# Kernel tuning notes

Hardware: AMD Instinct MI355X
Metric: run time of the kernel (lower is better)

The kernel has to match this reference:

```python
import jax, jax.numpy as jnp
import numpy as np
from jax import lax

WINDOW = 8
MAX_VAL = 1.0
C1 = (0.01 * MAX_VAL) ** 2
C2 = (0.03 * MAX_VAL) ** 2


def _box_sum(x):
    # Equivalent to conv2d with an all-ones WINDOW x WINDOW kernel, groups=C, VALID padding.
    return lax.reduce_window(x, 0.0, lax.add,
                             window_dimensions=(1, 1, WINDOW, WINDOW),
                             window_strides=(1, 1, 1, 1),
                             padding='VALID')


def setup_inputs() -> dict:
    key = jax.random.key(0)
    k1, k2 = jax.random.split(key)
    shape = (32, 3, 512, 512)  # NCHW, C=3 per groups=3 conv
    groundtruth = jax.random.uniform(k1, shape, dtype=jnp.float32)
    noisy_img = jax.random.uniform(k2, shape, dtype=jnp.float32)
    return {"groundtruth": groundtruth, "noisy_img": noisy_img}


def reference(groundtruth, noisy_img):
    mu1 = _box_sum(groundtruth)
    mu2 = _box_sum(noisy_img)
    mu1_sq = mu1 * mu1
    mu2_sq = mu2 * mu2
    mu1_mu2 = mu1 * mu2
    sigma1_sq = _box_sum(groundtruth * groundtruth) - mu1_sq
    sigma2_sq = _box_sum(noisy_img * noisy_img) - mu2_sq
    sigma12 = _box_sum(groundtruth * noisy_img) - mu1_mu2
    ssim_map = ((2.0 * mu1_mu2 + C1) * (2.0 * sigma12 + C2)) / (
        (mu1_sq + mu2_sq + C1) * (sigma1_sq + sigma2_sq + C2))
    return jnp.mean(1.0 - ssim_map)
```

## Files before the change

### kernel.cpp

```cpp
#include <hip/hip_runtime.h>


#define W 512
#define H 512
#define OW 505
#define OH 505
#define TH 16
#define NSTRIP ((OH + TH - 1) / TH)
#define NIMG 96
#define NPIX (96.0 * 505.0 * 505.0)

__device__ __forceinline__ float4 ld4(const float* p) { return *(const float4*)p; }
__device__ __forceinline__ float4 f4add(float4 a, float4 b) {
    return make_float4(a.x + b.x, a.y + b.y, a.z + b.z, a.w + b.w);
}
__device__ __forceinline__ float4 f4sub(float4 a, float4 b) {
    return make_float4(a.x - b.x, a.y - b.y, a.z - b.z, a.w - b.w);
}
__device__ __forceinline__ float4 f4mul(float4 a, float4 b) {
    return make_float4(a.x * b.x, a.y * b.y, a.z * b.z, a.w * b.w);
}

__global__ void finalize(const double* p, float* out) {
    out[0] = 1.0f - (float)(*p / NPIX);
}

__global__ void __launch_bounds__(128, 2)
ssim_main(const float* __restrict__ gt, const float* __restrict__ ni,
          double* __restrict__ acc_out)
{
    const int t   = threadIdx.x;
    const int c0  = t * 4;
    const int img = blockIdx.y;
    const int R0  = blockIdx.x * TH;
    const int R1  = min(R0 + TH, OH);

    const float C1 = 1e-4f;
    const float C2 = 9e-4f;

    const float* gx = gt + (size_t)img * (W * H) + c0;
    const float* gy = ni + (size_t)img * (W * H) + c0;

    __shared__ float vbuf[2][4][520];
    __shared__ float wpart[2];

    float4 ring_x[8], ring_y[8];
    float4 vsx = make_float4(0, 0, 0, 0);
    float4 vsy = make_float4(0, 0, 0, 0);
    float4 vsq = make_float4(0, 0, 0, 0);
    float4 vsp = make_float4(0, 0, 0, 0);

#pragma unroll
    for (int k = 0; k < 7; ++k) {
        float4 x = ld4(gx + (size_t)(R0 + k) * W);
        float4 y = ld4(gy + (size_t)(R0 + k) * W);
        ring_x[k] = x; ring_y[k] = y;
        vsx = f4add(vsx, x);
        vsy = f4add(vsy, y);
        vsq = f4add(vsq, f4add(f4mul(x, x), f4mul(y, y)));
        vsp = f4add(vsp, f4mul(x, y));
    }
    ring_x[7] = make_float4(0, 0, 0, 0);
    ring_y[7] = make_float4(0, 0, 0, 0);

    float4 px = ld4(gx + (size_t)(R0 + 7) * W);
    float4 py = ld4(gy + (size_t)(R0 + 7) * W);

    float acc = 0.0f;

#define HORIZ(q, v) {                                                     \
        float4 n1 = *(float4*)&vbuf[b][q][c0 + 4];                        \
        float4 n2 = *(float4*)&vbuf[b][q][c0 + 8];                        \
        float s = ((v.x + v.y) + (v.z + v.w)) +                           \
                  ((n1.x + n1.y) + (n1.z + n1.w));                        \
        B[q][0] = s;                                                      \
        s += n2.x - v.x; B[q][1] = s;                                     \
        s += n2.y - v.y; B[q][2] = s;                                     \
        s += n2.z - v.z; B[q][3] = s;                                     \
    }

#define ROWBODY(k, slot) {                                                \
        const int r = rbase + (k);                                        \
        if (r < R1) {                                  \
            float4 cx = px, cy = py;    \
            float4 ox = ring_x[slot], oy = ring_y[slot];                  \
            vsx = f4add(f4sub(vsx, ox), cx);                              \
            vsy = f4add(f4sub(vsy, oy), cy);                              \
            vsq = f4add(vsq, f4sub(f4add(f4mul(cx, cx), f4mul(cy, cy)),   \
                                   f4add(f4mul(ox, ox), f4mul(oy, oy)))); \
            vsp = f4add(vsp, f4sub(f4mul(cx, cy), f4mul(ox, oy)));        \
            ring_x[slot] = cx; ring_y[slot] = cy;                         \
            const int b = r & 1;                                          \
            *(float4*)&vbuf[b][0][c0] = vsx;                              \
            *(float4*)&vbuf[b][1][c0] = vsy;                              \
            *(float4*)&vbuf[b][2][c0] = vsq;                              \
            *(float4*)&vbuf[b][3][c0] = vsp;                              \
            __syncthreads();                                              \
            if (r + 1 < R1) {  \
                px = ld4(gx + (size_t)(r + 8) * W);                       \
                py = ld4(gy + (size_t)(r + 8) * W);                       \
            }                                                             \
            float B[4][4];                                                \
            HORIZ(0, vsx); HORIZ(1, vsy); HORIZ(2, vsq); HORIZ(3, vsp);   \
            _Pragma("unroll")                                             \
            for (int j = 0; j < 4; ++j) {                                 \
                float Sx = B[0][j], Sy = B[1][j];                         \
                float Sq = B[2][j], Sp = B[3][j];                         \
                float mu12 = Sx * Sy;                                     \
                float n1v = 2.0f * mu12 + C1;                             \
                float n2v = 2.0f * (Sp - mu12) + C2;                      \
                float sx2 = Sx * Sx, sy2 = Sy * Sy;                       \
                float d1  = sx2 + sy2 + C1;                               \
                float d2  = (Sq - sx2 - sy2) + C2;                        \
                float sv  = (n1v * n2v) * __builtin_amdgcn_rcpf(d1 * d2); \
                if (c0 + j < OW) acc += sv;                               \
            }                                                             \
        }                                                                 \
    }

    for (int rbase = R0; rbase < R1; rbase += 8) {
        ROWBODY(0, 7)
        ROWBODY(1, 0)
        ROWBODY(2, 1)
        ROWBODY(3, 2)
        ROWBODY(4, 3)
        ROWBODY(5, 4)
        ROWBODY(6, 5)
        ROWBODY(7, 6)
    }

#pragma unroll
    for (int off = 32; off > 0; off >>= 1) acc += __shfl_down(acc, off);
    const int wave = t >> 6, lane = t & 63;
    if (lane == 0) wpart[wave] = acc;
    __syncthreads();
    if (t == 0) atomicAdd(acc_out, (double)(wpart[0] + wpart[1]));
}

extern "C" void kernel_launch(void* const* d_in, const int* in_sizes, int n_in,
                              void* d_out, int out_size, void* d_ws, size_t ws_size,
                              hipStream_t stream) {
    const float* gt = (const float*)d_in[0];
    const float* ni = (const float*)d_in[1];
    double* acc = (double*)d_ws;

    hipMemsetAsync(acc, 0, sizeof(double), stream);
    dim3 grid(NSTRIP, NIMG);
    ssim_main<<<grid, 128, 0, stream>>>(gt, ni, acc);
    finalize<<<1, 1, 0, stream>>>(acc, (float*)d_out);
}
```

Baseline: 232.9 us.

## Batch four rows per barrier and deepen global prefetch to four rows

Result: no change. 229.4 us (-1.5%).

```diff
diff --git a/kernel.cpp b/kernel.cpp
--- a/kernel.cpp
+++ b/kernel.cpp
@@ -41,7 +41,7 @@
     const float* gx = gt + (size_t)img * (W * H) + c0;
     const float* gy = ni + (size_t)img * (W * H) + c0;
 
-    __shared__ float vbuf[2][4][520];
+    __shared__ float vbuf[4][4][520];
     __shared__ float wpart[2];
 
     float4 ring_x[8], ring_y[8];
@@ -63,26 +63,18 @@
     ring_x[7] = make_float4(0, 0, 0, 0);
     ring_y[7] = make_float4(0, 0, 0, 0);
 
-    float4 px = ld4(gx + (size_t)(R0 + 7) * W);
-    float4 py = ld4(gy + (size_t)(R0 + 7) * W);
+    float4 pfx[4], pfy[4];
+#pragma unroll
+    for (int m = 0; m < 4; ++m) {
+        pfx[m] = ld4(gx + (size_t)(R0 + 7 + m) * W);
+        pfy[m] = ld4(gy + (size_t)(R0 + 7 + m) * W);
+    }
 
     float acc = 0.0f;
 
-#define HORIZ(q, v) {                                                     \
-        float4 n1 = *(float4*)&vbuf[b][q][c0 + 4];                        \
-        float4 n2 = *(float4*)&vbuf[b][q][c0 + 8];                        \
-        float s = ((v.x + v.y) + (v.z + v.w)) +                           \
-                  ((n1.x + n1.y) + (n1.z + n1.w));                        \
-        B[q][0] = s;                                                      \
-        s += n2.x - v.x; B[q][1] = s;                                     \
-        s += n2.y - v.y; B[q][2] = s;                                     \
-        s += n2.z - v.z; B[q][3] = s;                                     \
-    }
-
-#define ROWBODY(k, slot) {                                                \
-        const int r = rbase + (k);                                        \
-        if (r < R1) {                                  \
-            float4 cx = px, cy = py;    \
+#define PHASEA_ROW(rb, m, slot) {                                         \
+        if ((rb) + (m) < R1) {                         \
+            float4 cx = pfx[m], cy = pfy[m];                              \
             float4 ox = ring_x[slot], oy = ring_y[slot];                  \
             vsx = f4add(f4sub(vsx, ox), cx);                              \
             vsy = f4add(f4sub(vsy, oy), cy);                              \
@@ -90,18 +82,30 @@
                                    f4add(f4mul(ox, ox), f4mul(oy, oy)))); \
             vsp = f4add(vsp, f4sub(f4mul(cx, cy), f4mul(ox, oy)));        \
             ring_x[slot] = cx; ring_y[slot] = cy;                         \
-            const int b = r & 1;                                          \
-            *(float4*)&vbuf[b][0][c0] = vsx;                              \
-            *(float4*)&vbuf[b][1][c0] = vsy;                              \
-            *(float4*)&vbuf[b][2][c0] = vsq;                              \
-            *(float4*)&vbuf[b][3][c0] = vsp;                              \
-            __syncthreads();                                              \
-            if (r + 1 < R1) {  \
-                px = ld4(gx + (size_t)(r + 8) * W);                       \
-                py = ld4(gy + (size_t)(r + 8) * W);                       \
-            }                                                             \
+            *(float4*)&vbuf[m][0][c0] = vsx;                              \
+            *(float4*)&vbuf[m][1][c0] = vsy;                              \
+            *(float4*)&vbuf[m][2][c0] = vsq;                              \
+            *(float4*)&vbuf[m][3][c0] = vsp;                              \
+        }                                                                 \
+    }
+
+#define HORIZ(q) {                                                        \
+        float4 o = *(float4*)&vbuf[m][q][c0];                             \
+        float4 a = *(float4*)&vbuf[m][q][c0 + 4];                         \
+        float4 e = *(float4*)&vbuf[m][q][c0 + 8];                         \
+        float s = ((o.x + o.y) + (o.z + o.w)) +                           \
+                  ((a.x + a.y) + (a.z + a.w));                            \
+        B[q][0] = s;                                                      \
+        s += e.x - o.x; B[q][1] = s;                                      \
+        s += e.y - o.y; B[q][2] = s;                                      \
+        s += e.z - o.z; B[q][3] = s;                                      \
+    }
+
+#define PHASEB_ROW(rb, mm) {                                              \
+        if ((rb) + (mm) < R1) {                        \
+            const int m = (mm);                                           \
             float B[4][4];                                                \
-            HORIZ(0, vsx); HORIZ(1, vsy); HORIZ(2, vsq); HORIZ(3, vsp);   \
+            HORIZ(0) HORIZ(1) HORIZ(2) HORIZ(3)                           \
             _Pragma("unroll")                                             \
             for (int j = 0; j < 4; ++j) {                                 \
                 float Sx = B[0][j], Sy = B[1][j];                         \
@@ -118,15 +122,27 @@
         }                                                                 \
     }
 
-    for (int rbase = R0; rbase < R1; rbase += 8) {
-        ROWBODY(0, 7)
-        ROWBODY(1, 0)
-        ROWBODY(2, 1)
-        ROWBODY(3, 2)
-        ROWBODY(4, 3)
-        ROWBODY(5, 4)
-        ROWBODY(6, 5)
-        ROWBODY(7, 6)
+#define GROUP(rb, s0, s1, s2, s3) {                                       \
+        if ((rb) < R1) {                               \
+            PHASEA_ROW(rb, 0, s0) PHASEA_ROW(rb, 1, s1)                   \
+            PHASEA_ROW(rb, 2, s2) PHASEA_ROW(rb, 3, s3)                   \
+            __syncthreads();                                              \
+            _Pragma("unroll")                                             \
+            for (int m = 0; m < 4; ++m) {      \
+                if ((rb) + 4 + m < R1) {                                  \
+                    pfx[m] = ld4(gx + (size_t)((rb) + 11 + m) * W);       \
+                    pfy[m] = ld4(gy + (size_t)((rb) + 11 + m) * W);       \
+                }                                                         \
+            }                                                             \
+            PHASEB_ROW(rb, 0) PHASEB_ROW(rb, 1)                           \
+            PHASEB_ROW(rb, 2) PHASEB_ROW(rb, 3)                           \
+            __syncthreads();                                              \
+        }                                                                 \
+    }
+
+    for (int rb0 = R0; rb0 < R1; rb0 += 8) {
+        GROUP(rb0,     7, 0, 1, 2)
+        GROUP(rb0 + 4, 3, 4, 5, 6)
     }
 
 #pragma unroll
```

## Replace shared-memory horizontal pass with redundant per-thread loads and horizontal-first sums

Applied to the files above, without the earlier changes.

Result: slower. 288.9 us (+24.0%).

```diff
diff --git a/kernel.cpp b/kernel.cpp
--- a/kernel.cpp
+++ b/kernel.cpp
@@ -2,7 +2,6 @@
 
 
 #define W 512
-#define H 512
 #define OW 505
 #define OH 505
 #define TH 16
@@ -11,101 +10,94 @@
 #define NPIX (96.0 * 505.0 * 505.0)
 
 __device__ __forceinline__ float4 ld4(const float* p) { return *(const float4*)p; }
-__device__ __forceinline__ float4 f4add(float4 a, float4 b) {
-    return make_float4(a.x + b.x, a.y + b.y, a.z + b.z, a.w + b.w);
-}
-__device__ __forceinline__ float4 f4sub(float4 a, float4 b) {
-    return make_float4(a.x - b.x, a.y - b.y, a.z - b.z, a.w - b.w);
-}
-__device__ __forceinline__ float4 f4mul(float4 a, float4 b) {
-    return make_float4(a.x * b.x, a.y * b.y, a.z * b.z, a.w * b.w);
-}
 
 __global__ void finalize(const double* p, float* out) {
     out[0] = 1.0f - (float)(*p / NPIX);
 }
 
-__global__ void __launch_bounds__(128, 2)
+__global__ void __launch_bounds__(128, 1)
 ssim_main(const float* __restrict__ gt, const float* __restrict__ ni,
           double* __restrict__ acc_out)
 {
     const int t   = threadIdx.x;
     const int c0  = t * 4;
+    const int c4  = (c0 + 4 < 508) ? c0 + 4 : 508;
+    const int c8  = (c0 + 8 < 508) ? c0 + 8 : 508;
     const int img = blockIdx.y;
     const int R0  = blockIdx.x * TH;
     const int R1  = min(R0 + TH, OH);
 
-    const float C1 = 1e-4f;
-    const float C2 = 9e-4f;
+    const float C1 = 1e-4f, C2 = 9e-4f;
 
-    const float* gx = gt + (size_t)img * (W * H) + c0;
-    const float* gy = ni + (size_t)img * (W * H) + c0;
+    const float* gx = gt + (size_t)img * (W * W);
+    const float* gy = ni + (size_t)img * (W * W);
 
-    __shared__ float vbuf[2][4][520];
     __shared__ float wpart[2];
 
-    float4 ring_x[8], ring_y[8];
-    float4 vsx = make_float4(0, 0, 0, 0);
-    float4 vsy = make_float4(0, 0, 0, 0);
-    float4 vsq = make_float4(0, 0, 0, 0);
-    float4 vsp = make_float4(0, 0, 0, 0);
+    float rgx[8][4], rgy[8][4], rgq[8][4], rgp[8][4];
+    float vsx[4], vsy[4], vsq[4], vsp[4];
+#pragma unroll
+    for (int j = 0; j < 4; ++j) { vsx[j]=0.f; vsy[j]=0.f; vsq[j]=0.f; vsp[j]=0.f; }
 
-#pragma unroll
-    for (int k = 0; k < 7; ++k) {
-        float4 x = ld4(gx + (size_t)(R0 + k) * W);
-        float4 y = ld4(gy + (size_t)(R0 + k) * W);
-        ring_x[k] = x; ring_y[k] = y;
-        vsx = f4add(vsx, x);
-        vsy = f4add(vsy, y);
-        vsq = f4add(vsq, f4add(f4mul(x, x), f4mul(y, y)));
-        vsp = f4add(vsp, f4mul(x, y));
-    }
-    ring_x[7] = make_float4(0, 0, 0, 0);
-    ring_y[7] = make_float4(0, 0, 0, 0);
+    float4 pf[2][6];
 
-    float4 px = ld4(gx + (size_t)(R0 + 7) * W);
-    float4 py = ld4(gy + (size_t)(R0 + 7) * W);
-
-    float acc = 0.0f;
-
-#define HORIZ(q, v) {                                                     \
-        float4 n1 = *(float4*)&vbuf[b][q][c0 + 4];                        \
-        float4 n2 = *(float4*)&vbuf[b][q][c0 + 8];                        \
-        float s = ((v.x + v.y) + (v.z + v.w)) +                           \
-                  ((n1.x + n1.y) + (n1.z + n1.w));                        \
-        B[q][0] = s;                                                      \
-        s += n2.x - v.x; B[q][1] = s;                                     \
-        s += n2.y - v.y; B[q][2] = s;                                     \
-        s += n2.z - v.z; B[q][3] = s;                                     \
+#define ISSUE(pp, row) {                                                  \
+        const float* bx_ = gx + (size_t)(row) * W;                        \
+        const float* by_ = gy + (size_t)(row) * W;                        \
+        pf[pp][0] = ld4(bx_ + c0); pf[pp][1] = ld4(bx_ + c4);             \
+        pf[pp][2] = ld4(bx_ + c8);                                        \
+        pf[pp][3] = ld4(by_ + c0); pf[pp][4] = ld4(by_ + c4);             \
+        pf[pp][5] = ld4(by_ + c8);                                        \
     }
 
-#define ROWBODY(k, slot) {                                                \
-        const int r = rbase + (k);                                        \
-        if (r < R1) {                                  \
-            float4 cx = px, cy = py;    \
-            float4 ox = ring_x[slot], oy = ring_y[slot];                  \
-            vsx = f4add(f4sub(vsx, ox), cx);                              \
-            vsy = f4add(f4sub(vsy, oy), cy);                              \
-            vsq = f4add(vsq, f4sub(f4add(f4mul(cx, cx), f4mul(cy, cy)),   \
-                                   f4add(f4mul(ox, ox), f4mul(oy, oy)))); \
-            vsp = f4add(vsp, f4sub(f4mul(cx, cy), f4mul(ox, oy)));        \
-            ring_x[slot] = cx; ring_y[slot] = cy;                         \
-            const int b = r & 1;                                          \
-            *(float4*)&vbuf[b][0][c0] = vsx;                              \
-            *(float4*)&vbuf[b][1][c0] = vsy;                              \
-            *(float4*)&vbuf[b][2][c0] = vsq;                              \
-            *(float4*)&vbuf[b][3][c0] = vsp;                              \
-            __syncthreads();                                              \
-            if (r + 1 < R1) {  \
-                px = ld4(gx + (size_t)(r + 8) * W);                       \
-                py = ld4(gy + (size_t)(r + 8) * W);                       \
+#define HS(Hd, v) {                                                       \
+        float s_ = ((v[0]+v[1])+(v[2]+v[3])) + ((v[4]+v[5])+(v[6]+v[7])); \
+        Hd[0] = s_;                                                       \
+        s_ += v[8]  - v[0]; Hd[1] = s_;                                   \
+        s_ += v[9]  - v[1]; Hd[2] = s_;                                   \
+        s_ += v[10] - v[2]; Hd[3] = s_;                                   \
+    }
+
+#define COMPH(pp, Hx, Hy, Hq, Hp) {                                       \
+        float x_[12], y_[12];                                             \
+        *(float4*)&x_[0] = pf[pp][0]; *(float4*)&x_[4] = pf[pp][1];       \
+        *(float4*)&x_[8] = pf[pp][2];                                     \
+        *(float4*)&y_[0] = pf[pp][3]; *(float4*)&y_[4] = pf[pp][4];       \
+        *(float4*)&y_[8] = pf[pp][5];                                     \
+        float q_[11], p_[11];                                             \
+        _Pragma("unroll") for (int i = 0; i < 11; ++i) {                  \
+            q_[i] = x_[i]*x_[i] + y_[i]*y_[i];                            \
+            p_[i] = x_[i]*y_[i];                                          \
+        }                                                                 \
+        HS(Hx, x_) HS(Hy, y_) HS(Hq, q_) HS(Hp, p_)                       \
+    }
+
+#define WARM(k) {                                                         \
+        float Hx[4], Hy[4], Hq[4], Hp[4];                                 \
+        COMPH((k)&1, Hx, Hy, Hq, Hp)                                      \
+        ISSUE((k)&1, R0 + (k) + 2)                                        \
+        _Pragma("unroll") for (int j = 0; j < 4; ++j) {                   \
+            rgx[k][j]=Hx[j]; rgy[k][j]=Hy[j];                             \
+            rgq[k][j]=Hq[j]; rgp[k][j]=Hp[j];                             \
+            vsx[j]+=Hx[j]; vsy[j]+=Hy[j]; vsq[j]+=Hq[j]; vsp[j]+=Hp[j];   \
+        }                                                                 \
+    }
+
+#define ROWB(k, slot) {                                                   \
+        const int r_ = rbase + (k);                                       \
+        if (r_ < R1) {                                 \
+            float Hx[4], Hy[4], Hq[4], Hp[4];                             \
+            COMPH(((k)+1)&1, Hx, Hy, Hq, Hp)                              \
+            if (r_ + 2 < R1) ISSUE(((k)+1)&1, r_ + 9)                     \
+            _Pragma("unroll") for (int j = 0; j < 4; ++j) {               \
+                vsx[j] += Hx[j] - rgx[slot][j]; rgx[slot][j] = Hx[j];     \
+                vsy[j] += Hy[j] - rgy[slot][j]; rgy[slot][j] = Hy[j];     \
+                vsq[j] += Hq[j] - rgq[slot][j]; rgq[slot][j] = Hq[j];     \
+                vsp[j] += Hp[j] - rgp[slot][j]; rgp[slot][j] = Hp[j];     \
             }                                                             \
-            float B[4][4];                                                \
-            HORIZ(0, vsx); HORIZ(1, vsy); HORIZ(2, vsq); HORIZ(3, vsp);   \
-            _Pragma("unroll")                                             \
-            for (int j = 0; j < 4; ++j) {                                 \
-                float Sx = B[0][j], Sy = B[1][j];                         \
-                float Sq = B[2][j], Sp = B[3][j];                         \
+            _Pragma("unroll") for (int j = 0; j < 4; ++j) {               \
+                float Sx = vsx[j], Sy = vsy[j];                           \
+                float Sq = vsq[j], Sp = vsp[j];                           \
                 float mu12 = Sx * Sy;                                     \
                 float n1v = 2.0f * mu12 + C1;                             \
                 float n2v = 2.0f * (Sp - mu12) + C2;                      \
@@ -118,15 +110,26 @@
         }                                                                 \
     }
 
+    ISSUE(0, R0)
+    ISSUE(1, R0 + 1)
+
+    WARM(0) WARM(1) WARM(2) WARM(3) WARM(4) WARM(5) WARM(6)
+#pragma unroll
+    for (int j = 0; j < 4; ++j) {
+        rgx[7][j]=0.f; rgy[7][j]=0.f; rgq[7][j]=0.f; rgp[7][j]=0.f;
+    }
+
+    float acc = 0.0f;
+
     for (int rbase = R0; rbase < R1; rbase += 8) {
-        ROWBODY(0, 7)
-        ROWBODY(1, 0)
-        ROWBODY(2, 1)
-        ROWBODY(3, 2)
-        ROWBODY(4, 3)
-        ROWBODY(5, 4)
-        ROWBODY(6, 5)
-        ROWBODY(7, 6)
+        ROWB(0, 7)
+        ROWB(1, 0)
+        ROWB(2, 1)
+        ROWB(3, 2)
+        ROWB(4, 3)
+        ROWB(5, 4)
+        ROWB(6, 5)
+        ROWB(7, 6)
     }
 
 #pragma unroll
```
